# Kernel optimization log

Measured on AMD Instinct MI355X. Metric: run time of the kernel, lower is better.

## Reference

```python
import jax, jax.numpy as jnp
import numpy as np

THRESH1 = 0.8      # snn.Leaky threshold
THRESH2 = 1.0      # snn.Synaptic default threshold
FS_SLOPE = 25.0    # surrogate.fast_sigmoid default slope
ATAN_ALPHA = 2.0   # surrogate.atan default alpha
TIME_STEPS = 20

# --- surrogate-gradient spike fns (forward = Heaviside) ---
@jax.custom_vjp
def spike_fs(x):
    return (x > 0).astype(x.dtype)
def _fs_fwd(x):
    return (x > 0).astype(x.dtype), x
def _fs_bwd(res, g):
    return (g / (FS_SLOPE * jnp.abs(res) + 1.0) ** 2,)
spike_fs.defvjp(_fs_fwd, _fs_bwd)

@jax.custom_vjp
def spike_atan(x):
    return (x > 0).astype(x.dtype)
def _at_fwd(x):
    return (x > 0).astype(x.dtype), x
def _at_bwd(res, g):
    return (g * (ATAN_ALPHA / 2.0) / (1.0 + (jnp.pi / 2.0 * ATAN_ALPHA * res) ** 2),)
spike_atan.defvjp(_at_fwd, _at_bwd)


def setup_inputs() -> dict:
    key = jax.random.key(0)
    ks = jax.random.split(key, 4)
    V, E, H, B, S = 32000, 256, 512, 8, 16
    x = jax.random.randint(ks[0], (B, S), 0, V)
    embed = jax.random.normal(ks[1], (V, E), jnp.float32)
    W1 = jax.random.normal(ks[2], (H, E), jnp.float32) / jnp.sqrt(jnp.float32(E))
    b1 = jnp.zeros((H,), jnp.float32)
    W2 = jax.random.normal(ks[3], (V, H), jnp.float32) / jnp.sqrt(jnp.float32(H))
    b2 = jnp.zeros((V,), jnp.float32)
    return dict(x=x, embed=embed, W1=W1, b1=b1, W2=W2, b2=b2,
                beta1=jnp.float32(0.85), alpha2=jnp.float32(0.9), beta2=jnp.float32(0.8))


def _forward(x, embed, W1, b1, W2, b2, beta1, alpha2, beta2):
    B, S = x.shape
    V, H = W2.shape
    b1c = jnp.clip(beta1, 0.0, 1.0)   # snntorch clamps learnable decays
    a2c = jnp.clip(alpha2, 0.0, 1.0)
    b2c = jnp.clip(beta2, 0.0, 1.0)
    # cur1 = fc1(embed(x[:, t])) is constant within the inner time loop
    cur1_all = jnp.einsum('bse,he->bsh', embed[x], W1) + b1  # (B, S, H)

    def seq_step(carry, cur1_t):              # cur1_t: (B, H)
        mem1, syn2, mem2 = carry

        def time_step(c, _):
            mem1, syn2, mem2, _ = c
            # Leaky: reset (subtract) from PREVIOUS mem, detached
            reset1 = jax.lax.stop_gradient((mem1 - THRESH1 > 0).astype(mem1.dtype))
            mem1 = b1c * mem1 + cur1_t - reset1 * THRESH1
            spk1 = spike_fs(mem1 - THRESH1)
            cur2 = spk1 @ W2.T + b2            # (B, V)
            # Synaptic: syn = a*syn + cur; mem = b*mem + syn - reset*thr
            reset2 = jax.lax.stop_gradient((mem2 - THRESH2 > 0).astype(mem2.dtype))
            syn2 = a2c * syn2 + cur2
            mem2 = b2c * mem2 + syn2 - reset2 * THRESH2
            spk2 = spike_atan(mem2 - THRESH2)
            return (mem1, syn2, mem2, spk2), None

        spk2_init = jnp.zeros_like(mem2)
        (mem1, syn2, mem2, spk2), _ = jax.lax.scan(
            time_step, (mem1, syn2, mem2, spk2_init), None, length=TIME_STEPS)
        return (mem1, syn2, mem2), spk2       # only last inner spk2 is emitted

    mem1 = jnp.zeros((B, H), jnp.float32)
    syn2 = jnp.zeros((B, V), jnp.float32)
    mem2 = jnp.zeros((B, V), jnp.float32)
    (mem1, syn2, mem2), outs = jax.lax.scan(
        seq_step, (mem1, syn2, mem2), jnp.swapaxes(cur1_all, 0, 1))
    return jnp.swapaxes(outs, 0, 1), mem1, syn2, mem2   # (B, S, V), states


def reference(x, embed, W1, b1, W2, b2, beta1, alpha2, beta2):
    return _forward(x, embed, W1, b1, W2, b2, beta1, alpha2, beta2)
```

## Files before the change

### kernel.cpp

```cpp
#include <hip/hip_runtime.h>
#include <cstdint>

constexpr int NV = 32000;
constexpr int NE = 256;
constexpr int NH = 512;
constexpr int NB = 8;
constexpr int NS = 16;
constexpr int NT = 20;
constexpr float TH1 = 0.8f;
constexpr float TH2 = 1.0f;

typedef _Float16 f16x8 __attribute__((ext_vector_type(8)));
typedef float f32x4 __attribute__((ext_vector_type(4)));

__device__ inline float clip01(float v) { return fminf(fmaxf(v, 0.f), 1.f); }

__device__ inline void bar_lds() {
  asm volatile("s_waitcnt lgkmcnt(0)" ::: "memory");
  __builtin_amdgcn_s_barrier();
  __builtin_amdgcn_sched_barrier(0);
}

__global__ void k_cur1(const int* __restrict__ x, const float* __restrict__ embed,
                       const float* __restrict__ W1, const float* __restrict__ b1,
                       float* __restrict__ cur1) {
  __shared__ float e[NE];
  int bs = blockIdx.x;
  int row = x[bs];
  e[threadIdx.x] = embed[(size_t)row * NE + threadIdx.x];
  __syncthreads();
  for (int hh = 0; hh < 2; ++hh) {
    int h = threadIdx.x + hh * 256;
    const float* w = W1 + (size_t)h * NE;
    float acc = 0.f;
#pragma unroll 8
    for (int k = 0; k < NE; ++k) acc = fmaf(e[k], w[k], acc);
    cur1[(size_t)bs * NH + h] = acc + b1[h];
  }
}

__global__ void k_spk1(const float* __restrict__ cur1, const float* __restrict__ pbeta1,
                       _Float16* __restrict__ A2F, float* __restrict__ mem1_out) {
  int g = blockIdx.x * blockDim.x + threadIdx.x;
  int b = g >> 9, h = g & 511;
  float bc = clip01(pbeta1[0]);
  float mem = 0.f;
  const _Float16 one  = (_Float16)1.0f;
  const _Float16 zero = (_Float16)0.0f;
  const int kfi = h >> 5;
  const int lhi = (h & 31) >> 3;
  const int e   = h & 7;
  for (int s = 0; s < NS; ++s) {
    float c = cur1[((size_t)b * NS + s) * NH + h];
    for (int t = 0; t < NT; ++t) {
      float rst = (mem > TH1) ? TH1 : 0.f;
      mem = __fsub_rn(__fadd_rn(__fmul_rn(bc, mem), c), rst);
      bool spk = mem > TH1;
      int gs = s * NT + t;
      int row = (gs & 7) * 8 + b;
      int lane = lhi * 16 + (row & 15);
      size_t addr = ((((size_t)(gs >> 3) * 16 + kfi) * 4 + (row >> 4)) * 64 + lane) * 8 + e;
      A2F[addr] = spk ? one : zero;
    }
  }
  mem1_out[g] = mem;
}

__global__ __launch_bounds__(1024, 4) void k_fused(
    const _Float16* __restrict__ A2F,
    const float* __restrict__ W2,
    const float* __restrict__ b2,
    const float* __restrict__ pa2, const float* __restrict__ pb2,
    float* __restrict__ out) {
  __shared__ float Cl[2][2][64 * 132];

  const int tid  = threadIdx.x;
  const int lane = tid & 63;
  const int wid  = tid >> 6;
  const int kh   = wid >> 3;
  const int wm   = (wid >> 2) & 1;
  const int wn   = wid & 3;
  const int n0   = blockIdx.x * 128;

  const int lr  = lane & 15;
  const int lk8 = (lane >> 4) * 8;
  const int cr  = (lane >> 4) * 4, cc = lane & 15;

  f16x8 bfr[2][8];
#pragma unroll
  for (int ni = 0; ni < 2; ++ni) {
    const int n = n0 + wn * 32 + ni * 16 + lr;
    const float* wp = W2 + (size_t)n * NH;
#pragma unroll
    for (int p = 0; p < 4; ++p) {
#pragma unroll
      for (int kf = 0; kf < 2; ++kf) {
        const int k0 = (kh * 4 + p) * 64 + kf * 32 + lk8;
        const float4 wa = *(const float4*)(wp + k0);
        const float4 wb = *(const float4*)(wp + k0 + 4);
        f16x8 v;
        v[0] = (_Float16)wa.x; v[1] = (_Float16)wa.y;
        v[2] = (_Float16)wa.z; v[3] = (_Float16)wa.w;
        v[4] = (_Float16)wb.x; v[5] = (_Float16)wb.y;
        v[6] = (_Float16)wb.z; v[7] = (_Float16)wb.w;
        bfr[ni][p * 2 + kf] = v;
      }
    }
  }

  const float a2  = clip01(pa2[0]);
  const float bcl = clip01(pb2[0]);
  const int vv = tid & 127;
  const int bb = tid >> 7;
  const float b2v = b2[n0 + vv];
  float syn = 0.f, mem = 0.f;
  unsigned spkmask = 0;
  f32x4 acc[2][2] = {};

  const _Float16* pAW = A2F + (size_t)kh * 16384 + wm * 1024 + lane * 8;

  f16x8 x0, x1, x2, x3, y0, y1, y2, y3;

#define LOADC(MT, P, S0, S1, S2, S3)                                          \
  {                                                                           \
    const _Float16* fb = pAW + (size_t)(MT) * 32768 + (P) * 4096;             \
    S0 = *(const f16x8*)(fb);                                    \
    S1 = *(const f16x8*)(fb + 512);                              \
    S2 = *(const f16x8*)(fb + 2048);                             \
    S3 = *(const f16x8*)(fb + 2560);                             \
  }

#define MFMAC(P, S0, S1, S2, S3)                                              \
  {                                                                           \
    acc[0][0] = __builtin_amdgcn_mfma_f32_16x16x32_f16(S0, bfr[0][(P)*2], acc[0][0], 0, 0, 0); \
    acc[1][0] = __builtin_amdgcn_mfma_f32_16x16x32_f16(S1, bfr[0][(P)*2], acc[1][0], 0, 0, 0); \
    acc[0][1] = __builtin_amdgcn_mfma_f32_16x16x32_f16(S0, bfr[1][(P)*2], acc[0][1], 0, 0, 0); \
    acc[1][1] = __builtin_amdgcn_mfma_f32_16x16x32_f16(S1, bfr[1][(P)*2], acc[1][1], 0, 0, 0); \
    acc[0][0] = __builtin_amdgcn_mfma_f32_16x16x32_f16(S2, bfr[0][(P)*2+1], acc[0][0], 0, 0, 0); \
    acc[1][0] = __builtin_amdgcn_mfma_f32_16x16x32_f16(S3, bfr[0][(P)*2+1], acc[1][0], 0, 0, 0); \
    acc[0][1] = __builtin_amdgcn_mfma_f32_16x16x32_f16(S2, bfr[1][(P)*2+1], acc[0][1], 0, 0, 0); \
    acc[1][1] = __builtin_amdgcn_mfma_f32_16x16x32_f16(S3, bfr[1][(P)*2+1], acc[1][1], 0, 0, 0); \
  }

  auto recur = [&](int mtq) {
    const float* C0 = Cl[mtq & 1][0];
    const float* C1 = Cl[mtq & 1][1];
#pragma unroll
    for (int st = 0; st < 8; ++st) {
      const int gs = mtq * 8 + st;
      const int idx = (st * 8 + bb) * 132 + vv;
      float cur2 = __fadd_rn(__fadd_rn(C0[idx], C1[idx]), b2v);
      float rst = (mem > TH2) ? 1.f : 0.f;
      syn = __fadd_rn(__fmul_rn(a2, syn), cur2);
      mem = __fsub_rn(__fadd_rn(__fmul_rn(bcl, mem), syn), rst);
      if (gs % 20 == 19)
        spkmask |= (mem > TH2 ? 1u : 0u) << (gs / 20);
    }
  };

  LOADC(0, 0, x0, x1, x2, x3);

  for (int mt = 0; mt < 40; ++mt) {
    LOADC(mt, 1, y0, y1, y2, y3);
    if (mt > 0) recur(mt - 1);
    __builtin_amdgcn_s_setprio(1);
    MFMAC(0, x0, x1, x2, x3);
    LOADC(mt, 2, x0, x1, x2, x3);  MFMAC(1, y0, y1, y2, y3);
    LOADC(mt, 3, y0, y1, y2, y3);  MFMAC(2, x0, x1, x2, x3);
    if (mt < 39) LOADC(mt + 1, 0, x0, x1, x2, x3);
    MFMAC(3, y0, y1, y2, y3);
    __builtin_amdgcn_s_setprio(0);

    float* Cw = Cl[mt & 1][kh];
#pragma unroll
    for (int mi = 0; mi < 2; ++mi)
#pragma unroll
      for (int ni = 0; ni < 2; ++ni) {
#pragma unroll
        for (int j = 0; j < 4; ++j)
          Cw[(wm * 32 + mi * 16 + cr + j) * 132 + wn * 32 + ni * 16 + cc] = acc[mi][ni][j];
        acc[mi][ni] = (f32x4){0.f, 0.f, 0.f, 0.f};
      }
    bar_lds();
  }
  recur(39);
#undef LOADC
#undef MFMAC

#pragma unroll
  for (int s = 0; s < NS; ++s)
    out[((size_t)bb * NS + s) * NV + n0 + vv] = (spkmask >> s) & 1 ? 1.f : 0.f;
  out[(size_t)4100096 + (size_t)bb * NV + n0 + vv] = syn;
  out[(size_t)4356096 + (size_t)bb * NV + n0 + vv] = mem;
}

extern "C" void kernel_launch(void* const* d_in, const int* in_sizes, int n_in,
                              void* d_out, int out_size, void* d_ws, size_t ws_size,
                              hipStream_t stream) {
  const int*   x     = (const int*)d_in[0];
  const float* embed = (const float*)d_in[1];
  const float* W1    = (const float*)d_in[2];
  const float* b1    = (const float*)d_in[3];
  const float* W2    = (const float*)d_in[4];
  const float* b2    = (const float*)d_in[5];
  const float* pb1   = (const float*)d_in[6];
  const float* pa2   = (const float*)d_in[7];
  const float* pb2   = (const float*)d_in[8];
  float* out = (float*)d_out;

  char* ws = (char*)d_ws;
  float* cur1 = (float*)ws;
  _Float16* A2F = (_Float16*)(ws + 262144);

  hipLaunchKernelGGL(k_cur1, dim3(NB * NS), dim3(256), 0, stream, x, embed, W1, b1, cur1);
  hipLaunchKernelGGL(k_spk1, dim3(16), dim3(256), 0, stream, cur1, pb1, A2F, out + 4096000);
  hipLaunchKernelGGL(k_fused, dim3(NV / 128), dim3(1024), 0, stream,
                     A2F, W2, b2, pa2, pb2, out);
}
```

Baseline: 156.3 us.

## Halve per-block vocab tile to 64 columns and rewarp the MFMA partition

The fused spike/recurrence kernel now covers 64 vocab columns per block instead of 128, which doubles the grid to 500 blocks. The 16 waves are regrouped as 2 K-halves × 4 M-tiles × 2 N-tiles, and each wave streams 8 K-fragments of A with a deeper software pipeline. The aim is to fill the GPU better, since 250 blocks under-occupy the CUs. In exchange, the A spike matrix is reread twice as many times overall, and only half the threads do the recurrence and output stores.

```diff
diff --git a/kernel.cpp b/kernel.cpp
--- a/kernel.cpp
+++ b/kernel.cpp
@@ -72,15 +72,15 @@
     const float* __restrict__ b2,
     const float* __restrict__ pa2, const float* __restrict__ pb2,
     float* __restrict__ out) {
-  __shared__ float Cl[2][2][64 * 132];
+  __shared__ float Cl[2][2][64 * 66];
 
   const int tid  = threadIdx.x;
   const int lane = tid & 63;
   const int wid  = tid >> 6;
-  const int kh   = wid >> 3;
-  const int wm   = (wid >> 2) & 1;
-  const int wn   = wid & 3;
-  const int n0   = blockIdx.x * 128;
+  const int kq   = wid >> 3;
+  const int wm   = (wid >> 1) & 3;
+  const int wn   = wid & 1;
+  const int n0   = blockIdx.x * 64;
 
   const int lr  = lane & 15;
   const int lk8 = (lane >> 4) * 8;
@@ -88,110 +88,99 @@
 
   f16x8 bfr[2][8];
 #pragma unroll
-  for (int ni = 0; ni < 2; ++ni) {
-    const int n = n0 + wn * 32 + ni * 16 + lr;
-    const float* wp = W2 + (size_t)n * NH;
-#pragma unroll
-    for (int p = 0; p < 4; ++p) {
-#pragma unroll
-      for (int kf = 0; kf < 2; ++kf) {
-        const int k0 = (kh * 4 + p) * 64 + kf * 32 + lk8;
-        const float4 wa = *(const float4*)(wp + k0);
-        const float4 wb = *(const float4*)(wp + k0 + 4);
-        f16x8 v;
-        v[0] = (_Float16)wa.x; v[1] = (_Float16)wa.y;
-        v[2] = (_Float16)wa.z; v[3] = (_Float16)wa.w;
-        v[4] = (_Float16)wb.x; v[5] = (_Float16)wb.y;
-        v[6] = (_Float16)wb.z; v[7] = (_Float16)wb.w;
-        bfr[ni][p * 2 + kf] = v;
-      }
+  for (int nf = 0; nf < 2; ++nf) {
+    const int n = n0 + wn * 32 + nf * 16 + lr;
+    const float* wp = W2 + (size_t)n * NH + kq * 256;
+#pragma unroll
+    for (int kf = 0; kf < 8; ++kf) {
+      const float4 wa = *(const float4*)(wp + kf * 32 + lk8);
+      const float4 wb = *(const float4*)(wp + kf * 32 + lk8 + 4);
+      f16x8 v;
+      v[0] = (_Float16)wa.x; v[1] = (_Float16)wa.y;
+      v[2] = (_Float16)wa.z; v[3] = (_Float16)wa.w;
+      v[4] = (_Float16)wb.x; v[5] = (_Float16)wb.y;
+      v[6] = (_Float16)wb.z; v[7] = (_Float16)wb.w;
+      bfr[nf][kf] = v;
     }
   }
 
   const float a2  = clip01(pa2[0]);
   const float bcl = clip01(pb2[0]);
-  const int vv = tid & 127;
-  const int bb = tid >> 7;
+  const int vv = tid & 63;
+  const int bb = (tid >> 6) & 7;
   const float b2v = b2[n0 + vv];
   float syn = 0.f, mem = 0.f;
   unsigned spkmask = 0;
-  f32x4 acc[2][2] = {};
-
-  const _Float16* pAW = A2F + (size_t)kh * 16384 + wm * 1024 + lane * 8;
-
-  f16x8 x0, x1, x2, x3, y0, y1, y2, y3;
-
-#define LOADC(MT, P, S0, S1, S2, S3)                                          \
-  {                                                                           \
-    const _Float16* fb = pAW + (size_t)(MT) * 32768 + (P) * 4096;             \
-    S0 = *(const f16x8*)(fb);                                    \
-    S1 = *(const f16x8*)(fb + 512);                              \
-    S2 = *(const f16x8*)(fb + 2048);                             \
-    S3 = *(const f16x8*)(fb + 2560);                             \
-  }
-
-#define MFMAC(P, S0, S1, S2, S3)                                              \
-  {                                                                           \
-    acc[0][0] = __builtin_amdgcn_mfma_f32_16x16x32_f16(S0, bfr[0][(P)*2], acc[0][0], 0, 0, 0); \
-    acc[1][0] = __builtin_amdgcn_mfma_f32_16x16x32_f16(S1, bfr[0][(P)*2], acc[1][0], 0, 0, 0); \
-    acc[0][1] = __builtin_amdgcn_mfma_f32_16x16x32_f16(S0, bfr[1][(P)*2], acc[0][1], 0, 0, 0); \
-    acc[1][1] = __builtin_amdgcn_mfma_f32_16x16x32_f16(S1, bfr[1][(P)*2], acc[1][1], 0, 0, 0); \
-    acc[0][0] = __builtin_amdgcn_mfma_f32_16x16x32_f16(S2, bfr[0][(P)*2+1], acc[0][0], 0, 0, 0); \
-    acc[1][0] = __builtin_amdgcn_mfma_f32_16x16x32_f16(S3, bfr[0][(P)*2+1], acc[1][0], 0, 0, 0); \
-    acc[0][1] = __builtin_amdgcn_mfma_f32_16x16x32_f16(S2, bfr[1][(P)*2+1], acc[0][1], 0, 0, 0); \
-    acc[1][1] = __builtin_amdgcn_mfma_f32_16x16x32_f16(S3, bfr[1][(P)*2+1], acc[1][1], 0, 0, 0); \
+  f32x4 acc[2] = {};
+
+  const _Float16* pAW = A2F + (size_t)(kq * 8) * 2048 + wm * 512 + lane * 8;
+
+  f16x8 a0_, a1_, a2_, a3_;
+
+#define LD(SLOT, MT, KF) SLOT = *(const f16x8*)(pAW + (size_t)(MT) * 32768 + (KF) * 2048);
+#define FM(SLOT, KF)                                                               \
+  {                                                                                \
+    acc[0] = __builtin_amdgcn_mfma_f32_16x16x32_f16(SLOT, bfr[0][KF], acc[0], 0, 0, 0); \
+    acc[1] = __builtin_amdgcn_mfma_f32_16x16x32_f16(SLOT, bfr[1][KF], acc[1], 0, 0, 0); \
   }
 
   auto recur = [&](int mtq) {
-    const float* C0 = Cl[mtq & 1][0];
-    const float* C1 = Cl[mtq & 1][1];
-#pragma unroll
-    for (int st = 0; st < 8; ++st) {
-      const int gs = mtq * 8 + st;
-      const int idx = (st * 8 + bb) * 132 + vv;
-      float cur2 = __fadd_rn(__fadd_rn(C0[idx], C1[idx]), b2v);
-      float rst = (mem > TH2) ? 1.f : 0.f;
-      syn = __fadd_rn(__fmul_rn(a2, syn), cur2);
-      mem = __fsub_rn(__fadd_rn(__fmul_rn(bcl, mem), syn), rst);
-      if (gs % 20 == 19)
-        spkmask |= (mem > TH2 ? 1u : 0u) << (gs / 20);
+    if (tid < 512) {
+      const float* C0 = Cl[mtq & 1][0];
+      const float* C1 = Cl[mtq & 1][1];
+#pragma unroll
+      for (int st = 0; st < 8; ++st) {
+        const int gs = mtq * 8 + st;
+        const int idx = (st * 8 + bb) * 66 + vv;
+        float cur2 = __fadd_rn(__fadd_rn(C0[idx], C1[idx]), b2v);
+        float rst = (mem > TH2) ? 1.f : 0.f;
+        syn = __fadd_rn(__fmul_rn(a2, syn), cur2);
+        mem = __fsub_rn(__fadd_rn(__fmul_rn(bcl, mem), syn), rst);
+        if (gs % 20 == 19)
+          spkmask |= (mem > TH2 ? 1u : 0u) << (gs / 20);
+      }
     }
   };
 
-  LOADC(0, 0, x0, x1, x2, x3);
+  LD(a0_, 0, 0); LD(a1_, 0, 1);
 
   for (int mt = 0; mt < 40; ++mt) {
-    LOADC(mt, 1, y0, y1, y2, y3);
+    LD(a2_, mt, 2);
     if (mt > 0) recur(mt - 1);
     __builtin_amdgcn_s_setprio(1);
-    MFMAC(0, x0, x1, x2, x3);
-    LOADC(mt, 2, x0, x1, x2, x3);  MFMAC(1, y0, y1, y2, y3);
-    LOADC(mt, 3, y0, y1, y2, y3);  MFMAC(2, x0, x1, x2, x3);
-    if (mt < 39) LOADC(mt + 1, 0, x0, x1, x2, x3);
-    MFMAC(3, y0, y1, y2, y3);
+    FM(a0_, 0)
+    LD(a3_, mt, 3)  FM(a1_, 1)
+    LD(a0_, mt, 4)  FM(a2_, 2)
+    LD(a1_, mt, 5)  FM(a3_, 3)
+    LD(a2_, mt, 6)  FM(a0_, 4)
+    LD(a3_, mt, 7)  FM(a1_, 5)
+    if (mt < 39) { LD(a0_, mt + 1, 0) }
+    FM(a2_, 6)
+    if (mt < 39) { LD(a1_, mt + 1, 1) }
+    FM(a3_, 7)
     __builtin_amdgcn_s_setprio(0);
 
-    float* Cw = Cl[mt & 1][kh];
-#pragma unroll
-    for (int mi = 0; mi < 2; ++mi)
-#pragma unroll
-      for (int ni = 0; ni < 2; ++ni) {
-#pragma unroll
-        for (int j = 0; j < 4; ++j)
-          Cw[(wm * 32 + mi * 16 + cr + j) * 132 + wn * 32 + ni * 16 + cc] = acc[mi][ni][j];
-        acc[mi][ni] = (f32x4){0.f, 0.f, 0.f, 0.f};
-      }
+    float* Cw = Cl[mt & 1][kq];
+#pragma unroll
+    for (int nf = 0; nf < 2; ++nf) {
+#pragma unroll
+      for (int j = 0; j < 4; ++j)
+        Cw[(wm * 16 + cr + j) * 66 + wn * 32 + nf * 16 + cc] = acc[nf][j];
+      acc[nf] = (f32x4){0.f, 0.f, 0.f, 0.f};
+    }
     bar_lds();
   }
   recur(39);
-#undef LOADC
-#undef MFMAC
-
-#pragma unroll
-  for (int s = 0; s < NS; ++s)
-    out[((size_t)bb * NS + s) * NV + n0 + vv] = (spkmask >> s) & 1 ? 1.f : 0.f;
-  out[(size_t)4100096 + (size_t)bb * NV + n0 + vv] = syn;
-  out[(size_t)4356096 + (size_t)bb * NV + n0 + vv] = mem;
+#undef LD
+#undef FM
+
+  if (tid < 512) {
+#pragma unroll
+    for (int s = 0; s < NS; ++s)
+      out[((size_t)bb * NS + s) * NV + n0 + vv] = (spkmask >> s) & 1 ? 1.f : 0.f;
+    out[(size_t)4100096 + (size_t)bb * NV + n0 + vv] = syn;
+    out[(size_t)4356096 + (size_t)bb * NV + n0 + vv] = mem;
+  }
 }
 
 extern "C" void kernel_launch(void* const* d_in, const int* in_sizes, int n_in,
@@ -214,6 +203,6 @@
 
   hipLaunchKernelGGL(k_cur1, dim3(NB * NS), dim3(256), 0, stream, x, embed, W1, b1, cur1);
   hipLaunchKernelGGL(k_spk1, dim3(16), dim3(256), 0, stream, cur1, pb1, A2F, out + 4096000);
-  hipLaunchKernelGGL(k_fused, dim3(NV / 128), dim3(1024), 0, stream,
+  hipLaunchKernelGGL(k_fused, dim3(NV / 64), dim3(1024), 0, stream,
                      A2F, W2, b2, pa2, pb2, out);
 }
```

Measured after the change: 185.0 us. +18.4%, slower.

## Fuse fc1 and layer-1 spike kernels and reorder spike fragment layout

Applied to the files above, without the earlier changes.

Merges the embedding-gather/fc1 kernel and the layer-1 Leaky recurrence into one kernel, so the cur1 workspace round trip and one kernel launch go away. Each thread now computes all 16 sequence positions for one hidden unit, reading its W1 row with float4 loads. The fp16 spike matrix layout is changed so each lane's 8-element fragment is contiguous along K, and W2 fragment loading in the fused kernel is rewritten to match. The recurrence also batches its LDS reads before the dependent arithmetic. The front kernel runs on only 16 blocks with a long serial loop, so its latency may dominate.

```diff
diff --git a/kernel.cpp b/kernel.cpp
--- a/kernel.cpp
+++ b/kernel.cpp
@@ -21,49 +21,60 @@
   __builtin_amdgcn_sched_barrier(0);
 }
 
-__global__ void k_cur1(const int* __restrict__ x, const float* __restrict__ embed,
-                       const float* __restrict__ W1, const float* __restrict__ b1,
-                       float* __restrict__ cur1) {
-  __shared__ float e[NE];
-  int bs = blockIdx.x;
-  int row = x[bs];
-  e[threadIdx.x] = embed[(size_t)row * NE + threadIdx.x];
+__global__ __launch_bounds__(256) void k_front(
+    const int* __restrict__ x, const float* __restrict__ embed,
+    const float* __restrict__ W1, const float* __restrict__ b1,
+    const float* __restrict__ pbeta1,
+    _Float16* __restrict__ A2F, float* __restrict__ mem1_out) {
+  __shared__ float emb[16][256];
+  const int tid = threadIdx.x;
+  const int blk = blockIdx.x;
+  const int b   = blk >> 1;
+  const int h   = ((blk & 1) << 8) + tid;
+
+  for (int s = 0; s < 16; ++s) {
+    const int row = x[b * 16 + s];
+    emb[s][tid] = embed[(size_t)row * NE + tid];
+  }
   __syncthreads();
-  for (int hh = 0; hh < 2; ++hh) {
-    int h = threadIdx.x + hh * 256;
-    const float* w = W1 + (size_t)h * NE;
-    float acc = 0.f;
-#pragma unroll 8
-    for (int k = 0; k < NE; ++k) acc = fmaf(e[k], w[k], acc);
-    cur1[(size_t)bs * NH + h] = acc + b1[h];
-  }
-}
-
-__global__ void k_spk1(const float* __restrict__ cur1, const float* __restrict__ pbeta1,
-                       _Float16* __restrict__ A2F, float* __restrict__ mem1_out) {
-  int g = blockIdx.x * blockDim.x + threadIdx.x;
-  int b = g >> 9, h = g & 511;
-  float bc = clip01(pbeta1[0]);
+
+  float c[16];
+#pragma unroll
+  for (int s = 0; s < 16; ++s) c[s] = 0.f;
+  const float* w = W1 + (size_t)h * NE;
+  for (int e4 = 0; e4 < 64; ++e4) {
+    const float4 wv = *(const float4*)(w + e4 * 4);
+#pragma unroll
+    for (int s = 0; s < 16; ++s) {
+      const float4 ev = *(const float4*)&emb[s][e4 * 4];
+      c[s] = fmaf(wv.w, ev.w, fmaf(wv.z, ev.z, fmaf(wv.y, ev.y, fmaf(wv.x, ev.x, c[s]))));
+    }
+  }
+  const float bias = b1[h];
+#pragma unroll
+  for (int s = 0; s < 16; ++s) c[s] = c[s] + bias;
+
+  const float bc = clip01(pbeta1[0]);
+  const int kfi = h >> 5;
+  const int k31 = h & 31;
   float mem = 0.f;
   const _Float16 one  = (_Float16)1.0f;
   const _Float16 zero = (_Float16)0.0f;
-  const int kfi = h >> 5;
-  const int lhi = (h & 31) >> 3;
-  const int e   = h & 7;
-  for (int s = 0; s < NS; ++s) {
-    float c = cur1[((size_t)b * NS + s) * NH + h];
+#pragma unroll
+  for (int s = 0; s < 16; ++s) {
+    const float cs = c[s];
     for (int t = 0; t < NT; ++t) {
       float rst = (mem > TH1) ? TH1 : 0.f;
-      mem = __fsub_rn(__fadd_rn(__fmul_rn(bc, mem), c), rst);
+      mem = __fsub_rn(__fadd_rn(__fmul_rn(bc, mem), cs), rst);
       bool spk = mem > TH1;
-      int gs = s * NT + t;
-      int row = (gs & 7) * 8 + b;
-      int lane = lhi * 16 + (row & 15);
-      size_t addr = ((((size_t)(gs >> 3) * 16 + kfi) * 4 + (row >> 4)) * 64 + lane) * 8 + e;
+      const int gs  = s * NT + t;
+      const int row = (gs & 7) * 8 + b;
+      size_t addr = (((size_t)(gs >> 3) * 16 + kfi) * 4 + (row >> 4)) * 512
+                  + (row & 15) * 32 + k31;
       A2F[addr] = spk ? one : zero;
     }
   }
-  mem1_out[g] = mem;
+  mem1_out[b * NH + h] = mem;
 }
 
 __global__ __launch_bounds__(1024, 4) void k_fused(
@@ -77,7 +88,7 @@
   const int tid  = threadIdx.x;
   const int lane = tid & 63;
   const int wid  = tid >> 6;
-  const int kh   = wid >> 3;
+  const int kq   = wid >> 3;
   const int wm   = (wid >> 2) & 1;
   const int wn   = wid & 3;
   const int n0   = blockIdx.x * 128;
@@ -90,21 +101,17 @@
 #pragma unroll
   for (int ni = 0; ni < 2; ++ni) {
     const int n = n0 + wn * 32 + ni * 16 + lr;
-    const float* wp = W2 + (size_t)n * NH;
-#pragma unroll
-    for (int p = 0; p < 4; ++p) {
-#pragma unroll
-      for (int kf = 0; kf < 2; ++kf) {
-        const int k0 = (kh * 4 + p) * 64 + kf * 32 + lk8;
-        const float4 wa = *(const float4*)(wp + k0);
-        const float4 wb = *(const float4*)(wp + k0 + 4);
-        f16x8 v;
-        v[0] = (_Float16)wa.x; v[1] = (_Float16)wa.y;
-        v[2] = (_Float16)wa.z; v[3] = (_Float16)wa.w;
-        v[4] = (_Float16)wb.x; v[5] = (_Float16)wb.y;
-        v[6] = (_Float16)wb.z; v[7] = (_Float16)wb.w;
-        bfr[ni][p * 2 + kf] = v;
-      }
+    const float* wp = W2 + (size_t)n * NH + kq * 256;
+#pragma unroll
+    for (int kf = 0; kf < 8; ++kf) {
+      const float4 wa = *(const float4*)(wp + kf * 32 + lk8);
+      const float4 wb = *(const float4*)(wp + kf * 32 + lk8 + 4);
+      f16x8 v;
+      v[0] = (_Float16)wa.x; v[1] = (_Float16)wa.y;
+      v[2] = (_Float16)wa.z; v[3] = (_Float16)wa.w;
+      v[4] = (_Float16)wb.x; v[5] = (_Float16)wb.y;
+      v[6] = (_Float16)wb.z; v[7] = (_Float16)wb.w;
+      bfr[ni][kf] = v;
     }
   }
 
@@ -117,17 +124,17 @@
   unsigned spkmask = 0;
   f32x4 acc[2][2] = {};
 
-  const _Float16* pAW = A2F + (size_t)kh * 16384 + wm * 1024 + lane * 8;
+  const _Float16* pAW = A2F + (size_t)kq * 16384 + wm * 1024 + lr * 32 + lk8;
 
   f16x8 x0, x1, x2, x3, y0, y1, y2, y3;
 
 #define LOADC(MT, P, S0, S1, S2, S3)                                          \
   {                                                                           \
     const _Float16* fb = pAW + (size_t)(MT) * 32768 + (P) * 4096;             \
-    S0 = *(const f16x8*)(fb);                                    \
-    S1 = *(const f16x8*)(fb + 512);                              \
-    S2 = *(const f16x8*)(fb + 2048);                             \
-    S3 = *(const f16x8*)(fb + 2560);                             \
+    S0 = *(const f16x8*)(fb);                               \
+    S1 = *(const f16x8*)(fb + 512);                         \
+    S2 = *(const f16x8*)(fb + 2048);                        \
+    S3 = *(const f16x8*)(fb + 2560);                        \
   }
 
 #define MFMAC(P, S0, S1, S2, S3)                                              \
@@ -145,11 +152,17 @@
   auto recur = [&](int mtq) {
     const float* C0 = Cl[mtq & 1][0];
     const float* C1 = Cl[mtq & 1][1];
+    float v0[8], v1[8];
+#pragma unroll
+    for (int st = 0; st < 8; ++st) {
+      const int idx = (st * 8 + bb) * 132 + vv;
+      v0[st] = C0[idx];
+      v1[st] = C1[idx];
+    }
 #pragma unroll
     for (int st = 0; st < 8; ++st) {
       const int gs = mtq * 8 + st;
-      const int idx = (st * 8 + bb) * 132 + vv;
-      float cur2 = __fadd_rn(__fadd_rn(C0[idx], C1[idx]), b2v);
+      float cur2 = __fadd_rn(__fadd_rn(v0[st], v1[st]), b2v);
       float rst = (mem > TH2) ? 1.f : 0.f;
       syn = __fadd_rn(__fmul_rn(a2, syn), cur2);
       mem = __fsub_rn(__fadd_rn(__fmul_rn(bcl, mem), syn), rst);
@@ -171,7 +184,7 @@
     MFMAC(3, y0, y1, y2, y3);
     __builtin_amdgcn_s_setprio(0);
 
-    float* Cw = Cl[mt & 1][kh];
+    float* Cw = Cl[mt & 1][kq];
 #pragma unroll
     for (int mi = 0; mi < 2; ++mi)
 #pragma unroll
@@ -208,12 +221,10 @@
   const float* pb2   = (const float*)d_in[8];
   float* out = (float*)d_out;
 
-  char* ws = (char*)d_ws;
-  float* cur1 = (float*)ws;
-  _Float16* A2F = (_Float16*)(ws + 262144);
-
-  hipLaunchKernelGGL(k_cur1, dim3(NB * NS), dim3(256), 0, stream, x, embed, W1, b1, cur1);
-  hipLaunchKernelGGL(k_spk1, dim3(16), dim3(256), 0, stream, cur1, pb1, A2F, out + 4096000);
+  _Float16* A2F = (_Float16*)d_ws;
+
+  hipLaunchKernelGGL(k_front, dim3(16), dim3(256), 0, stream,
+                     x, embed, W1, b1, pb1, A2F, out + 4096000);
   hipLaunchKernelGGL(k_fused, dim3(NV / 128), dim3(1024), 0, stream,
                      A2F, W2, b2, pa2, pb2, out);
 }
```

After: 214.2 us. 37.1% more time.
